# Performance work log

Measured on AMD Instinct MI355X. Metric: run time of the kernel, lower is better.

Reference implementation:

```python
import jax, jax.numpy as jnp
import numpy as np

EPS = 1e-6
FEAT = 1024
HEADS = 16
HDIM = FEAT // HEADS
FF = 500


def setup_inputs() -> dict:
    key = jax.random.key(0)
    ks = jax.random.split(key, 12)
    B, S = 4, 2048
    inp = {
        "x": jax.random.normal(ks[0], (B, S, FEAT), jnp.float32),
        "mask": jax.random.randint(ks[1], (B, S, S), 0, 2, jnp.int32),
        "alpha1": jnp.ones((FEAT,), jnp.float32),
        "bias1": jnp.zeros((FEAT,), jnp.float32),
        "alpha2": jnp.ones((FEAT,), jnp.float32),
        "bias2": jnp.zeros((FEAT,), jnp.float32),
        "Wq": jax.random.normal(ks[2], (FEAT, FEAT), jnp.float32) * (1.0 / np.sqrt(FEAT)),
        "bq": jnp.zeros((FEAT,), jnp.float32),
        "Wk": jax.random.normal(ks[3], (FEAT, FEAT), jnp.float32) * (1.0 / np.sqrt(FEAT)),
        "bk": jnp.zeros((FEAT,), jnp.float32),
        "Wv": jax.random.normal(ks[4], (FEAT, FEAT), jnp.float32) * (1.0 / np.sqrt(FEAT)),
        "bv": jnp.zeros((FEAT,), jnp.float32),
        "Wo": jax.random.normal(ks[5], (FEAT, FEAT), jnp.float32) * (1.0 / np.sqrt(FEAT)),
        "bo": jnp.zeros((FEAT,), jnp.float32),
        "W1": jax.random.normal(ks[6], (FEAT, FF), jnp.float32) * (1.0 / np.sqrt(FEAT)),
        "b1": jnp.zeros((FF,), jnp.float32),
        "W2": jax.random.normal(ks[7], (FF, FEAT), jnp.float32) * (1.0 / np.sqrt(FF)),
        "b2": jnp.zeros((FEAT,), jnp.float32),
    }
    return inp


def _norm(x, alpha, bias):
    m = jnp.mean(x, axis=-1, keepdims=True)
    # torch.std uses Bessel's correction (ddof=1)
    s = jnp.std(x, axis=-1, keepdims=True, ddof=1)
    return alpha * (x - m) / (s + EPS) + bias


def _attn(x2, mask, Wq, bq, Wk, bk, Wv, bv, Wo, bo):
    B, S, _ = x2.shape
    q = (x2 @ Wq + bq).reshape(B, S, HEADS, HDIM)
    k = (x2 @ Wk + bk).reshape(B, S, HEADS, HDIM)
    v = (x2 @ Wv + bv).reshape(B, S, HEADS, HDIM)
    scores = jnp.einsum("bqhd,bkhd->bhqk", q, k) / np.sqrt(HDIM).astype(np.float32)
    # faithful to source: masked positions filled with -1e-09 (not -1e9)
    scores = jnp.where(mask[:, None, :, :] == 0, jnp.float32(-1e-09), scores)
    probs = jax.nn.softmax(scores, axis=-1)
    out = jnp.einsum("bhqk,bkhd->bqhd", probs, v).reshape(B, S, FEAT)
    return out @ Wo + bo


def reference(x, mask, alpha1, bias1, alpha2, bias2, Wq, bq, Wk, bk, Wv, bv, Wo, bo, W1, b1, W2, b2):
    x2 = _norm(x, alpha1, bias1)
    x = x + _attn(x2, mask, Wq, bq, Wk, bk, Wv, bv, Wo, bo)
    x2 = _norm(x, alpha2, bias2)
    h = jax.nn.elu(x2 @ W1 + b1)
    x = x + (h @ W2 + b2)
    return x
```

## Files before the change

### kernel.cpp

```cpp
#include <hip/hip_runtime.h>
#include <hip/hip_bf16.h>
#include <math.h>

#define BATCH 4
#define SEQ 2048
#define FEAT 1024
#define HEADS 16
#define HDIM 64
#define FF 500
#define FFP 512
#define ROWS (BATCH * SEQ)
#define QKVSTR 3072
#define AQ 128

typedef unsigned short ushortT;
typedef __attribute__((ext_vector_type(8))) short short8;
typedef __attribute__((ext_vector_type(4))) float floatx4;

#if defined(__has_builtin) && __has_builtin(__builtin_amdgcn_exp2f)
#define EXP2F(x) __builtin_amdgcn_exp2f(x)
#else
#define EXP2F(x) exp2f(x)
#endif

__device__ __forceinline__ unsigned short f2bf(float f) {
    unsigned int u = __builtin_bit_cast(unsigned int, f);
    u += 0x7fffu + ((u >> 16) & 1u);
    return (unsigned short)(u >> 16);
}
__device__ __forceinline__ float bf2f(short b) {
    unsigned int u = ((unsigned int)(unsigned short)b) << 16;
    return __builtin_bit_cast(float, u);
}

__device__ __forceinline__ void async16(void* lds, const void* g) {
    __builtin_amdgcn_global_load_lds(
        (const __attribute__((address_space(1))) unsigned int*)g,
        (__attribute__((address_space(3))) unsigned int*)lds, 16, 0, 0);
}

__global__ void prep_kernel(const float* __restrict__ Wq, const float* __restrict__ Wk,
                            const float* __restrict__ Wv, const float* __restrict__ Wo,
                            const float* __restrict__ W1, const float* __restrict__ W2,
                            const float* __restrict__ bq, const float* __restrict__ bk,
                            const float* __restrict__ bv, const float* __restrict__ b1,
                            ushortT* __restrict__ Wqkvt, ushortT* __restrict__ Wot,
                            ushortT* __restrict__ W1t, ushortT* __restrict__ W2t,
                            float* __restrict__ bqkv, float* __restrict__ b1p)
{
    const int t = blockIdx.x;
    const int tid = threadIdx.x;
    if (t == 1280) {
        for (int i = tid; i < QKVSTR; i += 256)
            bqkv[i] = (i < 1024) ? bq[i] : ((i < 2048) ? bk[i - 1024] : bv[i - 2048]);
        for (int i = tid; i < FFP; i += 256)
            b1p[i] = (i < FF) ? b1[i] : 0.0f;
        return;
    }
    const float* W; ushortT* Wt; int K, N, Kp, bx, by;
    if (t < 1024) {
        const int wi = t >> 8, lt = t & 255;
        bx = lt & 15; by = lt >> 4; K = FEAT; N = FEAT; Kp = FEAT;
        W  = (wi == 0) ? Wq : (wi == 1) ? Wk : (wi == 2) ? Wv : Wo;
        Wt = (wi == 3) ? Wot : (Wqkvt + (size_t)wi * FEAT * FEAT);
    } else if (t < 1152) {
        const int lt = t - 1024; bx = lt & 7; by = lt >> 3;
        K = FEAT; N = FF; Kp = FEAT; W = W1; Wt = W1t;
    } else {
        const int lt = t - 1152; bx = lt & 15; by = lt >> 4;
        K = FF; N = FEAT; Kp = FFP; W = W2; Wt = W2t;
    }

    __shared__ float T[64][65];
    const int n0 = bx * 64, k0 = by * 64;
    const int r = tid >> 4;
    const int c = (tid & 15) * 4;
    #pragma unroll
    for (int i = 0; i < 4; i++) {
        const int kk = k0 + r + i * 16;
        #pragma unroll
        for (int e = 0; e < 4; e++) {
            const int nn = n0 + c + e;
            T[r + i * 16][c + e] = (kk < K && nn < N) ? W[(size_t)kk * N + nn] : 0.0f;
        }
    }
    __syncthreads();
    #pragma unroll
    for (int i = 0; i < 4; i++) {
        const int nn = r + i * 16;
        ushort4 o;
        o.x = f2bf(T[c + 0][nn]);
        o.y = f2bf(T[c + 1][nn]);
        o.z = f2bf(T[c + 2][nn]);
        o.w = f2bf(T[c + 3][nn]);
        *(ushort4*)(Wt + (size_t)(n0 + nn) * Kp + k0 + c) = o;
    }
}

__global__ void maskbits_kernel(const int* __restrict__ mask,
                                unsigned int* __restrict__ bits)
{
    const size_t g = (size_t)blockIdx.x * 256 + threadIdx.x;
    const int lane = threadIdx.x & 63;
    const unsigned long long bal = __ballot(mask[g] != 0);
    if (lane == 0)  bits[g >> 5] = (unsigned int)bal;
    if (lane == 32) bits[g >> 5] = (unsigned int)(bal >> 32);
}

__global__ void ln_kernel(const float* __restrict__ x,
                          const float* __restrict__ alpha,
                          const float* __restrict__ bias,
                          ushortT* __restrict__ out)
{
    __shared__ float p1[4], p2[4];
    const int row = blockIdx.x;
    const int tid = threadIdx.x;
    const int wave = tid >> 6, lane = tid & 63;
    float4 v = ((const float4*)(x + (size_t)row * FEAT))[tid];

    float s1 = v.x + v.y + v.z + v.w;
    float s2 = v.x * v.x + v.y * v.y + v.z * v.z + v.w * v.w;
    #pragma unroll
    for (int off = 32; off > 0; off >>= 1) {
        s1 += __shfl_xor(s1, off);
        s2 += __shfl_xor(s2, off);
    }
    if (lane == 0) { p1[wave] = s1; p2[wave] = s2; }
    __syncthreads();
    const float t1 = p1[0] + p1[1] + p1[2] + p1[3];
    const float t2 = p2[0] + p2[1] + p2[2] + p2[3];
    const float mean = t1 * (1.0f / 1024.0f);
    const float var = fmaxf(t2 - 1024.0f * mean * mean, 0.0f) * (1.0f / 1023.0f);
    const float inv = 1.0f / (sqrtf(var) + 1e-6f);

    const float4 a = ((const float4*)alpha)[tid];
    const float4 b = ((const float4*)bias)[tid];
    ushort4 o;
    o.x = f2bf(a.x * (v.x - mean) * inv + b.x);
    o.y = f2bf(a.y * (v.y - mean) * inv + b.y);
    o.z = f2bf(a.z * (v.z - mean) * inv + b.z);
    o.w = f2bf(a.w * (v.w - mean) * inv + b.w);
    ((ushort4*)(out + (size_t)row * FEAT))[tid] = o;
}

template<int ACT, int RES, int OUT_BF16, int BN>
__global__ __launch_bounds__(256)
void mfma_gemm(const ushortT* __restrict__ A, const ushortT* __restrict__ Bt,
               const float* __restrict__ bias, const float* __restrict__ R,
               void* __restrict__ Cout, int M, int N, int K)
{
    constexpr int MT = (BN == 128) ? 4 : 2;
    constexpr int MSPAN = (BN == 128) ? 64 : 32;
    __shared__ ushortT As[2][128 * 32];
    __shared__ ushortT Bs[2][BN * 32];

    const int tid  = threadIdx.x;
    const int wave = tid >> 6, lane = tid & 63;
    const int quad = lane >> 4, l16 = lane & 15;
    const int wm = (BN == 128) ? (wave >> 1) : wave;
    const int wn = (BN == 128) ? (wave & 1) : 0;
    const int row0 = blockIdx.y * 128, col0 = blockIdx.x * BN;

    const floatx4 z4 = {0.f, 0.f, 0.f, 0.f};
    floatx4 acc[MT][4];
    #pragma unroll
    for (int i = 0; i < MT; i++)
        #pragma unroll
        for (int j = 0; j < 4; j++) acc[i][j] = z4;

    for (int k0 = 0; k0 < K; k0 += 64) {
        __syncthreads();
        #pragma unroll
        for (int kh = 0; kh < 2; kh++) {
            #pragma unroll
            for (int i = 0; i < 2; i++) {
                const int rbase = 16 * (wave + 4 * i);
                const int r = rbase + (lane >> 2);
                const int co = (lane & 3) * 8;
                async16((char*)As[kh] + rbase * 64,
                        A + (size_t)(row0 + r) * K + k0 + kh * 32 + co);
            }
            if (BN == 128) {
                #pragma unroll
                for (int i = 0; i < 2; i++) {
                    const int rbase = 16 * (wave + 4 * i);
                    const int r = rbase + (lane >> 2);
                    const int co = (lane & 3) * 8;
                    async16((char*)Bs[kh] + rbase * 64,
                            Bt + (size_t)(col0 + r) * K + k0 + kh * 32 + co);
                }
            } else {
                const int rbase = 16 * wave;
                const int r = rbase + (lane >> 2);
                const int co = (lane & 3) * 8;
                async16((char*)Bs[kh] + rbase * 64,
                        Bt + (size_t)(col0 + r) * K + k0 + kh * 32 + co);
            }
        }
        __syncthreads();

        #pragma unroll
        for (int kh = 0; kh < 2; kh++) {
            short8 af[MT], bf[4];
            #pragma unroll
            for (int mt = 0; mt < MT; mt++)
                af[mt] = *(const short8*)&As[kh][(MSPAN * wm + 16 * mt + l16) * 32 + quad * 8];
            #pragma unroll
            for (int nt = 0; nt < 4; nt++)
                bf[nt] = *(const short8*)&Bs[kh][(64 * wn + 16 * nt + l16) * 32 + quad * 8];
            #pragma unroll
            for (int mt = 0; mt < MT; mt++)
                #pragma unroll
                for (int nt = 0; nt < 4; nt++)
                    acc[mt][nt] = __builtin_amdgcn_mfma_f32_16x16x32_bf16(
                        af[mt], bf[nt], acc[mt][nt], 0, 0, 0);
        }
    }

    #pragma unroll
    for (int mt = 0; mt < MT; mt++) {
        #pragma unroll
        for (int nt = 0; nt < 4; nt++) {
            const int col = col0 + 64 * wn + 16 * nt + l16;
            #pragma unroll
            for (int r = 0; r < 4; r++) {
                const int row = row0 + MSPAN * wm + 16 * mt + quad * 4 + r;
                float val = acc[mt][nt][r] + bias[col];
                if (ACT == 1) val = (val > 0.0f) ? val : (__expf(val) - 1.0f);
                if (RES) val += R[(size_t)row * N + col];
                if (OUT_BF16)
                    ((ushortT*)Cout)[(size_t)row * N + col] = f2bf(val);
                else
                    ((float*)Cout)[(size_t)row * N + col] = val;
            }
        }
    }
}

__global__ void transpose_v_kernel(const ushortT* __restrict__ v, ushortT* __restrict__ vt)
{
    __shared__ ushortT T[64][80];
    const int bid = blockIdx.x;
    const int jt = bid & 31, h = (bid >> 5) & 15, b = bid >> 9;
    const int j0 = jt * 64;
    const int tid = threadIdx.x;

    const int j = tid >> 2;
    #pragma unroll
    for (int i = 0; i < 2; i++) {
        const int c = (tid & 3) * 2 + i;
        short8 val = *(const short8*)(v + (size_t)(b * SEQ + j0 + j) * QKVSTR + h * 64 + c * 8);
        *(short8*)&T[j][c * 8] = val;
    }
    __syncthreads();
    const int d = tid >> 2;
    #pragma unroll
    for (int i = 0; i < 2; i++) {
        const int cj = (tid & 3) * 2 + i;
        union { short8 v8; ushortT u[8]; } tmp;
        #pragma unroll
        for (int e = 0; e < 8; e++) tmp.u[e] = T[cj * 8 + e][d];
        *(short8*)(vt + ((size_t)((b * HEADS + h) * 64 + d)) * SEQ + j0 + cj * 8) = tmp.v8;
    }
}

__global__ __launch_bounds__(256)
void mfma_attn(const ushortT* __restrict__ qkv, const ushortT* __restrict__ vt,
               const unsigned int* __restrict__ mbits, ushortT* __restrict__ attn_out)
{
    __shared__ ushortT Ks[2][64 * 64];
    __shared__ ushortT Vts[2][64 * 64];
    __shared__ ushortT Ps[AQ * 64];

    const int tid = threadIdx.x;
    const int wave = tid >> 6, lane = tid & 63;
    const int quad = lane >> 4, l16 = lane & 15;
    const int bid = ((blockIdx.x & 7) << 7) | (blockIdx.x >> 3);
    const int qt = bid & 15, h = (bid >> 4) & 15, b = bid >> 8;
    const int q0 = qt * AQ;

    const ushortT* qptr = qkv;
    const ushortT* kptr = qkv + 1024;

    short8 qf[2][2];
    #pragma unroll
    for (int mg = 0; mg < 2; mg++) {
        const size_t qrow = (size_t)(b * SEQ + q0 + 32 * wave + mg * 16 + l16);
        short8 t0 = *(const short8*)(qptr + qrow * QKVSTR + h * 64 + quad * 8);
        short8 t1 = *(const short8*)(qptr + qrow * QKVSTR + h * 64 + 32 + quad * 8);
        const float cs = 0.125f * 1.4426950408889634f;
        #pragma unroll
        for (int i = 0; i < 8; i++) {
            qf[mg][0][i] = (short)f2bf(bf2f(t0[i]) * cs);
            qf[mg][1][i] = (short)f2bf(bf2f(t1[i]) * cs);
        }
    }

    short8 ones8;
    #pragma unroll
    for (int i = 0; i < 8; i++) ones8[i] = (short)0x3F80;

    const floatx4 z4 = {0.f, 0.f, 0.f, 0.f};
    floatx4 o[2][4];
    #pragma unroll
    for (int mg = 0; mg < 2; mg++)
        #pragma unroll
        for (int dt = 0; dt < 4; dt++) o[mg][dt] = z4;
    floatx4 lacc[2] = {z4, z4};

    const int rr = tid >> 2;
    const int c0 = (tid & 3) * 2;
    const ushortT* gk = kptr + (size_t)(b * SEQ + rr) * QKVSTR + h * 64;
    const ushortT* gv = vt + ((size_t)((b * HEADS + h) * 64 + rr)) * SEQ;
    short8 rk0, rk1, rv0, rv1;

#define ATTN_ISSUE() {                                                       \
    rk0 = *(const short8*)(gk + c0 * 8);                                     \
    rk1 = *(const short8*)(gk + c0 * 8 + 8);                                 \
    rv0 = *(const short8*)(gv + c0 * 8);                                     \
    rv1 = *(const short8*)(gv + c0 * 8 + 8);                                 \
    gk += (size_t)64 * QKVSTR; gv += 64; }

#define ATTN_WRITE(BI) {                                                     \
    *(short8*)&Ks[BI][rr * 64 + ((c0 ^ (rr & 7)) * 8)] = rk0;                \
    *(short8*)&Ks[BI][rr * 64 + (((c0 + 1) ^ (rr & 7)) * 8)] = rk1;          \
    *(short8*)&Vts[BI][rr * 64 + ((c0 ^ (rr & 7)) * 8)] = rv0;               \
    *(short8*)&Vts[BI][rr * 64 + (((c0 + 1) ^ (rr & 7)) * 8)] = rv1; }

    const unsigned int* mrowp[2];
    mrowp[0] = mbits + (size_t)(b * SEQ + q0 + 32 * wave + l16) * (SEQ / 32);
    mrowp[1] = mrowp[0] + 16 * (SEQ / 32);
    const int mloc0 = 32 * wave + l16;

    ATTN_ISSUE();
    ATTN_WRITE(0);
    unsigned int w[2][2];
    #pragma unroll
    for (int mg = 0; mg < 2; mg++) {
        w[mg][0] = mrowp[mg][0];
        w[mg][1] = mrowp[mg][1];
    }

    #pragma unroll 2
    for (int jt = 0; jt < 32; jt++) {
        __syncthreads();
        const int cur = jt & 1;
        unsigned int wn[2][2];
        if (jt < 31) {
            ATTN_ISSUE();
            #pragma unroll
            for (int mg = 0; mg < 2; mg++) {
                wn[mg][0] = mrowp[mg][jt * 2 + 2];
                wn[mg][1] = mrowp[mg][jt * 2 + 3];
            }
        }

        floatx4 st[2][4];
        __builtin_amdgcn_s_setprio(1);
        #pragma unroll
        for (int nt = 0; nt < 4; nt++) {
            const int j = nt * 16 + l16;
            short8 ka0 = *(const short8*)&Ks[cur][j * 64 + ((quad ^ (j & 7)) * 8)];
            short8 ka1 = *(const short8*)&Ks[cur][j * 64 + (((4 + quad) ^ (j & 7)) * 8)];
            #pragma unroll
            for (int mg = 0; mg < 2; mg++) {
                floatx4 t = z4;
                t = __builtin_amdgcn_mfma_f32_16x16x32_bf16(ka0, qf[mg][0], t, 0, 0, 0);
                t = __builtin_amdgcn_mfma_f32_16x16x32_bf16(ka1, qf[mg][1], t, 0, 0, 0);
                st[mg][nt] = t;
            }
        }
        __builtin_amdgcn_s_setprio(0);

        #pragma unroll
        for (int mg = 0; mg < 2; mg++) {
            const int mloc = mloc0 + mg * 16;
            #pragma unroll
            for (int nt = 0; nt < 4; nt++) {
                const unsigned int ww = (nt & 2) ? w[mg][1] : w[mg][0];
                const unsigned int wsh = ww >> ((nt & 1) * 16 + quad * 4);
                float p[4];
                p[0] = EXP2F((wsh & 1u) ? st[mg][nt][0] : 0.0f);
                p[1] = EXP2F((wsh & 2u) ? st[mg][nt][1] : 0.0f);
                p[2] = EXP2F((wsh & 4u) ? st[mg][nt][2] : 0.0f);
                p[3] = EXP2F((wsh & 8u) ? st[mg][nt][3] : 0.0f);
                const int j0 = nt * 16 + quad * 4;
                const int chunk = (j0 >> 3) ^ (mloc & 7);
                const int ci = j0 & 7;
                ushortT* dst = &Ps[mloc * 64 + chunk * 8 + ci];
                *(__hip_bfloat162*)(dst)     = __float22bfloat162_rn(make_float2(p[0], p[1]));
                *(__hip_bfloat162*)(dst + 2) = __float22bfloat162_rn(make_float2(p[2], p[3]));
            }
        }

        short8 pa[2][2];
        #pragma unroll
        for (int mg = 0; mg < 2; mg++) {
            const int mloc = mloc0 + mg * 16;
            pa[mg][0] = *(const short8*)&Ps[mloc * 64 + ((quad ^ (mloc & 7)) * 8)];
            pa[mg][1] = *(const short8*)&Ps[mloc * 64 + (((4 + quad) ^ (mloc & 7)) * 8)];
            lacc[mg] = __builtin_amdgcn_mfma_f32_16x16x32_bf16(pa[mg][0], ones8, lacc[mg], 0, 0, 0);
            lacc[mg] = __builtin_amdgcn_mfma_f32_16x16x32_bf16(pa[mg][1], ones8, lacc[mg], 0, 0, 0);
        }
        __builtin_amdgcn_s_setprio(1);
        #pragma unroll
        for (int dt = 0; dt < 4; dt++) {
            const int d = dt * 16 + l16;
            short8 vb0 = *(const short8*)&Vts[cur][d * 64 + ((quad ^ (d & 7)) * 8)];
            short8 vb1 = *(const short8*)&Vts[cur][d * 64 + (((4 + quad) ^ (d & 7)) * 8)];
            #pragma unroll
            for (int mg = 0; mg < 2; mg++) {
                o[mg][dt] = __builtin_amdgcn_mfma_f32_16x16x32_bf16(pa[mg][0], vb0, o[mg][dt], 0, 0, 0);
                o[mg][dt] = __builtin_amdgcn_mfma_f32_16x16x32_bf16(pa[mg][1], vb1, o[mg][dt], 0, 0, 0);
            }
        }
        __builtin_amdgcn_s_setprio(0);

        if (jt < 31) {
            ATTN_WRITE(cur ^ 1);
            #pragma unroll
            for (int mg = 0; mg < 2; mg++) {
                w[mg][0] = wn[mg][0];
                w[mg][1] = wn[mg][1];
            }
        }
    }

    #pragma unroll
    for (int mg = 0; mg < 2; mg++) {
        #pragma unroll
        for (int r = 0; r < 4; r++) {
            const float inv_l = 1.0f / lacc[mg][r];
            const size_t row = (size_t)(b * SEQ + q0 + 32 * wave + mg * 16 + quad * 4 + r);
            #pragma unroll
            for (int dt = 0; dt < 4; dt++) {
                attn_out[row * FEAT + h * 64 + dt * 16 + l16] = f2bf(o[mg][dt][r] * inv_l);
            }
        }
    }
#undef ATTN_ISSUE
#undef ATTN_WRITE
}

extern "C" void kernel_launch(void* const* d_in, const int* in_sizes, int n_in,
                              void* d_out, int out_size, void* d_ws, size_t ws_size,
                              hipStream_t stream)
{
    const float* x      = (const float*)d_in[0];
    const int*   mask   = (const int*)d_in[1];
    const float* alpha1 = (const float*)d_in[2];
    const float* bias1  = (const float*)d_in[3];
    const float* alpha2 = (const float*)d_in[4];
    const float* bias2  = (const float*)d_in[5];
    const float* Wq     = (const float*)d_in[6];
    const float* bq     = (const float*)d_in[7];
    const float* Wk     = (const float*)d_in[8];
    const float* bk     = (const float*)d_in[9];
    const float* Wv     = (const float*)d_in[10];
    const float* bv     = (const float*)d_in[11];
    const float* Wo     = (const float*)d_in[12];
    const float* bo     = (const float*)d_in[13];
    const float* W1     = (const float*)d_in[14];
    const float* b1     = (const float*)d_in[15];
    const float* W2     = (const float*)d_in[16];
    const float* b2     = (const float*)d_in[17];
    float* out = (float*)d_out;

    char* ws = (char*)d_ws;
    const size_t MB = 1024 * 1024;
    ushortT* x2b    = (ushortT*)(ws);
    ushortT* attn_o = (ushortT*)(ws);
    ushortT* qkv    = (ushortT*)(ws + 16 * MB);
    ushortT* x2b2   = (ushortT*)(ws + 16 * MB);
    ushortT* hbuf   = (ushortT*)(ws + 32 * MB);
    ushortT* vtb    = (ushortT*)(ws + 64 * MB);
    ushortT* Wqkvt  = (ushortT*)(ws + 80 * MB);
    ushortT* Wot    = (ushortT*)(ws + 86 * MB);
    ushortT* W1t    = (ushortT*)(ws + 88 * MB);
    ushortT* W2t    = (ushortT*)(ws + 89 * MB);
    float*   b1p    = (float*)  (ws + 90 * MB);
    float*   bqkv   = (float*)  (ws + 90 * MB + 16384);
    unsigned int* mbits = (unsigned int*)(ws + 91 * MB);

    const dim3 blk(256);

    prep_kernel<<<1281, blk, 0, stream>>>(Wq, Wk, Wv, Wo, W1, W2, bq, bk, bv, b1,
                                          Wqkvt, Wot, W1t, W2t, bqkv, b1p);
    maskbits_kernel<<<(BATCH * SEQ * SEQ) / 256, blk, 0, stream>>>(mask, mbits);

    ln_kernel<<<ROWS, blk, 0, stream>>>(x, alpha1, bias1, x2b);

    mfma_gemm<0, 0, 1, 128><<<dim3(24, 64), blk, 0, stream>>>(
        x2b, Wqkvt, bqkv, nullptr, qkv, ROWS, QKVSTR, FEAT);

    transpose_v_kernel<<<BATCH * HEADS * (SEQ / 64), blk, 0, stream>>>(qkv + 2048, vtb);
    mfma_attn<<<BATCH * HEADS * (SEQ / AQ), blk, 0, stream>>>(qkv, vtb, mbits, attn_o);

    mfma_gemm<0, 1, 0, 128><<<dim3(8, 64), blk, 0, stream>>>(
        attn_o, Wot, bo, x, out, ROWS, FEAT, FEAT);

    ln_kernel<<<ROWS, blk, 0, stream>>>(out, alpha2, bias2, x2b2);

    mfma_gemm<1, 0, 1, 64><<<dim3(FFP / 64, 64), blk, 0, stream>>>(
        x2b2, W1t, b1p, nullptr, hbuf, ROWS, FFP, FEAT);

    mfma_gemm<0, 1, 0, 128><<<dim3(8, 64), blk, 0, stream>>>(
        hbuf, W2t, b2, out, out, ROWS, FEAT, FFP);
}
```

Measured before the change: 466.5 us.

## Split attention query tile across eight waves with one 16-row group each

```diff
diff --git a/kernel.cpp b/kernel.cpp
--- a/kernel.cpp
+++ b/kernel.cpp
@@ -264,7 +264,7 @@
     }
 }
 
-__global__ __launch_bounds__(256)
+__global__ __launch_bounds__(512)
 void mfma_attn(const ushortT* __restrict__ qkv, const ushortT* __restrict__ vt,
                const unsigned int* __restrict__ mbits, ushortT* __restrict__ attn_out)
 {
@@ -282,17 +282,16 @@
     const ushortT* qptr = qkv;
     const ushortT* kptr = qkv + 1024;
 
-    short8 qf[2][2];
-    #pragma unroll
-    for (int mg = 0; mg < 2; mg++) {
-        const size_t qrow = (size_t)(b * SEQ + q0 + 32 * wave + mg * 16 + l16);
+    short8 qf[2];
+    {
+        const size_t qrow = (size_t)(b * SEQ + q0 + 16 * wave + l16);
         short8 t0 = *(const short8*)(qptr + qrow * QKVSTR + h * 64 + quad * 8);
         short8 t1 = *(const short8*)(qptr + qrow * QKVSTR + h * 64 + 32 + quad * 8);
         const float cs = 0.125f * 1.4426950408889634f;
         #pragma unroll
         for (int i = 0; i < 8; i++) {
-            qf[mg][0][i] = (short)f2bf(bf2f(t0[i]) * cs);
-            qf[mg][1][i] = (short)f2bf(bf2f(t1[i]) * cs);
+            qf[0][i] = (short)f2bf(bf2f(t0[i]) * cs);
+            qf[1][i] = (short)f2bf(bf2f(t1[i]) * cs);
         }
     }
 
@@ -301,141 +300,104 @@
     for (int i = 0; i < 8; i++) ones8[i] = (short)0x3F80;
 
     const floatx4 z4 = {0.f, 0.f, 0.f, 0.f};
-    floatx4 o[2][4];
-    #pragma unroll
-    for (int mg = 0; mg < 2; mg++)
-        #pragma unroll
-        for (int dt = 0; dt < 4; dt++) o[mg][dt] = z4;
-    floatx4 lacc[2] = {z4, z4};
-
-    const int rr = tid >> 2;
-    const int c0 = (tid & 3) * 2;
-    const ushortT* gk = kptr + (size_t)(b * SEQ + rr) * QKVSTR + h * 64;
-    const ushortT* gv = vt + ((size_t)((b * HEADS + h) * 64 + rr)) * SEQ;
-    short8 rk0, rk1, rv0, rv1;
+    floatx4 o[4];
+    #pragma unroll
+    for (int dt = 0; dt < 4; dt++) o[dt] = z4;
+    floatx4 lacc = z4;
+
+    const int rr = tid >> 3;
+    const int c0 = tid & 7;
+    const ushortT* gk = kptr + (size_t)(b * SEQ + rr) * QKVSTR + h * 64 + c0 * 8;
+    const ushortT* gv = vt + ((size_t)((b * HEADS + h) * 64 + rr)) * SEQ + c0 * 8;
+    short8 rk, rv;
 
 #define ATTN_ISSUE() {                                                       \
-    rk0 = *(const short8*)(gk + c0 * 8);                                     \
-    rk1 = *(const short8*)(gk + c0 * 8 + 8);                                 \
-    rv0 = *(const short8*)(gv + c0 * 8);                                     \
-    rv1 = *(const short8*)(gv + c0 * 8 + 8);                                 \
+    rk = *(const short8*)gk;                                                 \
+    rv = *(const short8*)gv;                                                 \
     gk += (size_t)64 * QKVSTR; gv += 64; }
 
 #define ATTN_WRITE(BI) {                                                     \
-    *(short8*)&Ks[BI][rr * 64 + ((c0 ^ (rr & 7)) * 8)] = rk0;                \
-    *(short8*)&Ks[BI][rr * 64 + (((c0 + 1) ^ (rr & 7)) * 8)] = rk1;          \
-    *(short8*)&Vts[BI][rr * 64 + ((c0 ^ (rr & 7)) * 8)] = rv0;               \
-    *(short8*)&Vts[BI][rr * 64 + (((c0 + 1) ^ (rr & 7)) * 8)] = rv1; }
-
-    const unsigned int* mrowp[2];
-    mrowp[0] = mbits + (size_t)(b * SEQ + q0 + 32 * wave + l16) * (SEQ / 32);
-    mrowp[1] = mrowp[0] + 16 * (SEQ / 32);
-    const int mloc0 = 32 * wave + l16;
+    *(short8*)&Ks[BI][rr * 64 + ((c0 ^ (rr & 7)) * 8)] = rk;                 \
+    *(short8*)&Vts[BI][rr * 64 + ((c0 ^ (rr & 7)) * 8)] = rv; }
+
+    const unsigned int* mrowp =
+        mbits + (size_t)(b * SEQ + q0 + 16 * wave + l16) * (SEQ / 32);
+    const int mloc = 16 * wave + l16;
 
     ATTN_ISSUE();
     ATTN_WRITE(0);
-    unsigned int w[2][2];
-    #pragma unroll
-    for (int mg = 0; mg < 2; mg++) {
-        w[mg][0] = mrowp[mg][0];
-        w[mg][1] = mrowp[mg][1];
-    }
+    unsigned int w0 = mrowp[0], w1 = mrowp[1];
 
     #pragma unroll 2
     for (int jt = 0; jt < 32; jt++) {
         __syncthreads();
         const int cur = jt & 1;
-        unsigned int wn[2][2];
+        unsigned int wn0, wn1;
         if (jt < 31) {
             ATTN_ISSUE();
-            #pragma unroll
-            for (int mg = 0; mg < 2; mg++) {
-                wn[mg][0] = mrowp[mg][jt * 2 + 2];
-                wn[mg][1] = mrowp[mg][jt * 2 + 3];
-            }
-        }
-
-        floatx4 st[2][4];
+            wn0 = mrowp[jt * 2 + 2];
+            wn1 = mrowp[jt * 2 + 3];
+        }
+
+        floatx4 st[4];
         __builtin_amdgcn_s_setprio(1);
         #pragma unroll
         for (int nt = 0; nt < 4; nt++) {
             const int j = nt * 16 + l16;
             short8 ka0 = *(const short8*)&Ks[cur][j * 64 + ((quad ^ (j & 7)) * 8)];
             short8 ka1 = *(const short8*)&Ks[cur][j * 64 + (((4 + quad) ^ (j & 7)) * 8)];
-            #pragma unroll
-            for (int mg = 0; mg < 2; mg++) {
-                floatx4 t = z4;
-                t = __builtin_amdgcn_mfma_f32_16x16x32_bf16(ka0, qf[mg][0], t, 0, 0, 0);
-                t = __builtin_amdgcn_mfma_f32_16x16x32_bf16(ka1, qf[mg][1], t, 0, 0, 0);
-                st[mg][nt] = t;
-            }
+            floatx4 t = z4;
+            t = __builtin_amdgcn_mfma_f32_16x16x32_bf16(ka0, qf[0], t, 0, 0, 0);
+            t = __builtin_amdgcn_mfma_f32_16x16x32_bf16(ka1, qf[1], t, 0, 0, 0);
+            st[nt] = t;
         }
         __builtin_amdgcn_s_setprio(0);
 
         #pragma unroll
-        for (int mg = 0; mg < 2; mg++) {
-            const int mloc = mloc0 + mg * 16;
-            #pragma unroll
-            for (int nt = 0; nt < 4; nt++) {
-                const unsigned int ww = (nt & 2) ? w[mg][1] : w[mg][0];
-                const unsigned int wsh = ww >> ((nt & 1) * 16 + quad * 4);
-                float p[4];
-                p[0] = EXP2F((wsh & 1u) ? st[mg][nt][0] : 0.0f);
-                p[1] = EXP2F((wsh & 2u) ? st[mg][nt][1] : 0.0f);
-                p[2] = EXP2F((wsh & 4u) ? st[mg][nt][2] : 0.0f);
-                p[3] = EXP2F((wsh & 8u) ? st[mg][nt][3] : 0.0f);
-                const int j0 = nt * 16 + quad * 4;
-                const int chunk = (j0 >> 3) ^ (mloc & 7);
-                const int ci = j0 & 7;
-                ushortT* dst = &Ps[mloc * 64 + chunk * 8 + ci];
-                *(__hip_bfloat162*)(dst)     = __float22bfloat162_rn(make_float2(p[0], p[1]));
-                *(__hip_bfloat162*)(dst + 2) = __float22bfloat162_rn(make_float2(p[2], p[3]));
-            }
-        }
-
-        short8 pa[2][2];
-        #pragma unroll
-        for (int mg = 0; mg < 2; mg++) {
-            const int mloc = mloc0 + mg * 16;
-            pa[mg][0] = *(const short8*)&Ps[mloc * 64 + ((quad ^ (mloc & 7)) * 8)];
-            pa[mg][1] = *(const short8*)&Ps[mloc * 64 + (((4 + quad) ^ (mloc & 7)) * 8)];
-            lacc[mg] = __builtin_amdgcn_mfma_f32_16x16x32_bf16(pa[mg][0], ones8, lacc[mg], 0, 0, 0);
-            lacc[mg] = __builtin_amdgcn_mfma_f32_16x16x32_bf16(pa[mg][1], ones8, lacc[mg], 0, 0, 0);
-        }
+        for (int nt = 0; nt < 4; nt++) {
+            const unsigned int ww = (nt & 2) ? w1 : w0;
+            const unsigned int wsh = ww >> ((nt & 1) * 16 + quad * 4);
+            float p[4];
+            p[0] = EXP2F((wsh & 1u) ? st[nt][0] : 0.0f);
+            p[1] = EXP2F((wsh & 2u) ? st[nt][1] : 0.0f);
+            p[2] = EXP2F((wsh & 4u) ? st[nt][2] : 0.0f);
+            p[3] = EXP2F((wsh & 8u) ? st[nt][3] : 0.0f);
+            const int j0 = nt * 16 + quad * 4;
+            const int chunk = (j0 >> 3) ^ (mloc & 7);
+            const int ci = j0 & 7;
+            ushortT* dst = &Ps[mloc * 64 + chunk * 8 + ci];
+            *(__hip_bfloat162*)(dst)     = __float22bfloat162_rn(make_float2(p[0], p[1]));
+            *(__hip_bfloat162*)(dst + 2) = __float22bfloat162_rn(make_float2(p[2], p[3]));
+        }
+
+        short8 pa0 = *(const short8*)&Ps[mloc * 64 + ((quad ^ (mloc & 7)) * 8)];
+        short8 pa1 = *(const short8*)&Ps[mloc * 64 + (((4 + quad) ^ (mloc & 7)) * 8)];
+        lacc = __builtin_amdgcn_mfma_f32_16x16x32_bf16(pa0, ones8, lacc, 0, 0, 0);
+        lacc = __builtin_amdgcn_mfma_f32_16x16x32_bf16(pa1, ones8, lacc, 0, 0, 0);
         __builtin_amdgcn_s_setprio(1);
         #pragma unroll
         for (int dt = 0; dt < 4; dt++) {
             const int d = dt * 16 + l16;
             short8 vb0 = *(const short8*)&Vts[cur][d * 64 + ((quad ^ (d & 7)) * 8)];
             short8 vb1 = *(const short8*)&Vts[cur][d * 64 + (((4 + quad) ^ (d & 7)) * 8)];
-            #pragma unroll
-            for (int mg = 0; mg < 2; mg++) {
-                o[mg][dt] = __builtin_amdgcn_mfma_f32_16x16x32_bf16(pa[mg][0], vb0, o[mg][dt], 0, 0, 0);
-                o[mg][dt] = __builtin_amdgcn_mfma_f32_16x16x32_bf16(pa[mg][1], vb1, o[mg][dt], 0, 0, 0);
-            }
+            o[dt] = __builtin_amdgcn_mfma_f32_16x16x32_bf16(pa0, vb0, o[dt], 0, 0, 0);
+            o[dt] = __builtin_amdgcn_mfma_f32_16x16x32_bf16(pa1, vb1, o[dt], 0, 0, 0);
         }
         __builtin_amdgcn_s_setprio(0);
 
         if (jt < 31) {
             ATTN_WRITE(cur ^ 1);
-            #pragma unroll
-            for (int mg = 0; mg < 2; mg++) {
-                w[mg][0] = wn[mg][0];
-                w[mg][1] = wn[mg][1];
-            }
-        }
-    }
-
-    #pragma unroll
-    for (int mg = 0; mg < 2; mg++) {
-        #pragma unroll
-        for (int r = 0; r < 4; r++) {
-            const float inv_l = 1.0f / lacc[mg][r];
-            const size_t row = (size_t)(b * SEQ + q0 + 32 * wave + mg * 16 + quad * 4 + r);
-            #pragma unroll
-            for (int dt = 0; dt < 4; dt++) {
-                attn_out[row * FEAT + h * 64 + dt * 16 + l16] = f2bf(o[mg][dt][r] * inv_l);
-            }
+            w0 = wn0; w1 = wn1;
+        }
+    }
+
+    #pragma unroll
+    for (int r = 0; r < 4; r++) {
+        const float inv_l = 1.0f / lacc[r];
+        const size_t row = (size_t)(b * SEQ + q0 + 16 * wave + quad * 4 + r);
+        #pragma unroll
+        for (int dt = 0; dt < 4; dt++) {
+            attn_out[row * FEAT + h * 64 + dt * 16 + l16] = f2bf(o[dt][r] * inv_l);
         }
     }
 #undef ATTN_ISSUE
@@ -494,7 +456,7 @@
         x2b, Wqkvt, bqkv, nullptr, qkv, ROWS, QKVSTR, FEAT);
 
     transpose_v_kernel<<<BATCH * HEADS * (SEQ / 64), blk, 0, stream>>>(qkv + 2048, vtb);
-    mfma_attn<<<BATCH * HEADS * (SEQ / AQ), blk, 0, stream>>>(qkv, vtb, mbits, attn_o);
+    mfma_attn<<<BATCH * HEADS * (SEQ / AQ), dim3(512), 0, stream>>>(qkv, vtb, mbits, attn_o);
 
     mfma_gemm<0, 1, 0, 128><<<dim3(8, 64), blk, 0, stream>>>(
         attn_o, Wot, bo, x, out, ROWS, FEAT, FEAT);
```

Result: no change. 459.6 us (-1.5%).
